# Performance work log

Hardware: AMD Instinct MI355X
Metric: run time of the kernel (lower is better)

The kernel has to match this reference:

```python
import jax, jax.numpy as jnp
import numpy as np

B, T, D, H, V = 512, 128, 1024, 1024, 256
STEPS = 26  # batch_max_length (25) + 1


def setup_inputs() -> dict:
    key = jax.random.key(0)
    ks = jax.random.split(key, 12)
    s = lambda *sh: 1.0 / np.sqrt(sh[-1])
    inp = {
        "batch_H": jax.random.normal(ks[0], (B, T, D), dtype=jnp.float32),
        "text": jax.random.randint(ks[1], (B, STEPS), 0, V, dtype=jnp.int64),
        # AttentionCell params
        "i2h_w": jax.random.normal(ks[2], (H, D), dtype=jnp.float32) * s(H, D),
        "h2h_w": jax.random.normal(ks[3], (H, H), dtype=jnp.float32) * s(H, H),
        "h2h_b": jnp.zeros((H,), dtype=jnp.float32),
        "score_w": jax.random.normal(ks[4], (1, H), dtype=jnp.float32) * s(1, H),
        # LSTMCell params (input = context[D] ++ onehot[V])
        "W_ih": jax.random.normal(ks[5], (4 * H, D + V), dtype=jnp.float32) * s(4 * H, D + V),
        "W_hh": jax.random.normal(ks[6], (4 * H, H), dtype=jnp.float32) * s(4 * H, H),
        "b_ih": jnp.zeros((4 * H,), dtype=jnp.float32),
        "b_hh": jnp.zeros((4 * H,), dtype=jnp.float32),
        # generator
        "gen_w": jax.random.normal(ks[7], (V, H), dtype=jnp.float32) * s(V, H),
        "gen_b": jnp.zeros((V,), dtype=jnp.float32),
    }
    return inp


def reference(batch_H, text, i2h_w, h2h_w, h2h_b, score_w, W_ih, W_hh, b_ih, b_hh, gen_w, gen_b):
    # proj_H = i2h(batch_H): step-invariant, hoisted out of the loop (same math)
    proj_H = jnp.einsum("btd,hd->bth", batch_H, i2h_w)  # [B,T,H]
    dtype = batch_H.dtype

    def step(carry, tok):
        h, c = carry
        # Bahdanau additive attention
        proj_h = h @ h2h_w.T + h2h_b                       # [B,H]
        e = jnp.tanh(proj_H + proj_h[:, None, :]) @ score_w[0]  # [B,T]
        alpha = jax.nn.softmax(e, axis=1)                   # [B,T]
        context = jnp.einsum("bt,btd->bd", alpha, batch_H)  # [B,D]
        x = jnp.concatenate([context, jax.nn.one_hot(tok, V, dtype=dtype)], axis=1)
        # LSTMCell (torch gate order: i, f, g, o)
        gates = x @ W_ih.T + b_ih + h @ W_hh.T + b_hh       # [B,4H]
        i_g, f_g, g_g, o_g = jnp.split(gates, 4, axis=1)
        c_new = jax.nn.sigmoid(f_g) * c + jax.nn.sigmoid(i_g) * jnp.tanh(g_g)
        h_new = jax.nn.sigmoid(o_g) * jnp.tanh(c_new)
        return (h_new, c_new), h_new

    h0 = jnp.zeros((B, H), dtype=dtype)
    c0 = jnp.zeros((B, H), dtype=dtype)
    tokens = jnp.swapaxes(text[:, :STEPS], 0, 1)            # [STEPS,B]
    _, out_hid = jax.lax.scan(step, (h0, c0), tokens)       # [STEPS,B,H]
    out_hid = jnp.swapaxes(out_hid, 0, 1)                   # [B,STEPS,H]
    logits = jnp.einsum("bsh,vh->bsv", out_hid, gen_w) + gen_b
    return logits  # [B, STEPS, V]
```

## Files before the change

kernel.cpp:

```cpp
#include <hip/hip_runtime.h>
#include <hip/hip_fp16.h>

#define BB 512
#define TT 128
#define DD 1024
#define HH 1024
#define VV 256
#define SS 26

typedef _Float16 half8 __attribute__((ext_vector_type(8)));
typedef _Float16 half4 __attribute__((ext_vector_type(4)));
typedef float f32x4 __attribute__((ext_vector_type(4)));

__device__ __forceinline__ void cp16(const void* g, void* l) {
    __builtin_amdgcn_global_load_lds(
        (const __attribute__((address_space(1))) void*)g,
        (__attribute__((address_space(3))) void*)l, 16, 0, 0);
}

__device__ __forceinline__ float tanh_fast(float x) {
    float ex = __expf(2.f * x);
    return 1.f - 2.f * __builtin_amdgcn_rcpf(ex + 1.f);
}
__device__ __forceinline__ float sigmoid_fast(float x) {
    return __builtin_amdgcn_rcpf(1.f + __expf(-x));
}

__global__ void cvt_f32_to_f16_v4(const float* __restrict__ src,
                                  _Float16* __restrict__ dst, long n4) {
    long i = (long)blockIdx.x * blockDim.x + threadIdx.x;
    long stride = (long)gridDim.x * blockDim.x;
    for (; i < n4; i += stride) {
        float4 v = ((const float4*)src)[i];
        half4 h;
        h[0] = (_Float16)v.x; h[1] = (_Float16)v.y;
        h[2] = (_Float16)v.z; h[3] = (_Float16)v.w;
        ((half4*)dst)[i] = h;
    }
}

__global__ void build_wcatp(const float* __restrict__ W_ih,
                            const float* __restrict__ W_hh,
                            _Float16* __restrict__ wcatp) {
    int idx = blockIdx.x * 256 + threadIdx.x;
    int c = idx >> 11;
    int k = idx & 2047;
    int g = c >> 6, q = (c >> 4) & 3, jl = c & 15;
    int row = q * 1024 + g * 16 + jl;
    float v = (k < 1024) ? W_ih[(size_t)row * 1280 + k]
                         : W_hh[(size_t)row * 1024 + (k - 1024)];
    wcatp[idx] = (_Float16)v;
}

__global__ void build_onehT(const float* __restrict__ W_ih,
                            float* __restrict__ onehT) {
    int idx = blockIdx.x * 256 + threadIdx.x;
    int v = idx >> 12;
    int g = idx & 4095;
    onehT[idx] = W_ih[(size_t)g * 1280 + 1024 + v];
}

__global__ void build_bsum(const float* __restrict__ b_ih,
                           const float* __restrict__ b_hh,
                           float* __restrict__ bsum) {
    int i = blockIdx.x * 256 + threadIdx.x;
    bsum[i] = b_ih[i] + b_hh[i];
}

template <int MODE, int SWZ>
__global__ __launch_bounds__(256) void gemm_bt(
    const _Float16* __restrict__ A, int lda,
    const _Float16* __restrict__ B, int ldb,
    void* __restrict__ Cp, int ldc, int K, const float* __restrict__ bias) {
    __shared__ __align__(16) _Float16 As[2][128 * 32];
    __shared__ __align__(16) _Float16 Bs[2][128 * 32];

    int bx = blockIdx.x, by = blockIdx.y;
    if (SWZ) {
        int nx = gridDim.x;
        int bid = by * nx + bx;
        int xcd = bid & 7;
        int local = bid >> 3;
        int rows_per_xcd = gridDim.y >> 3;
        bx = local % nx;
        by = xcd * rows_per_xcd + local / nx;
    }
    const int tid  = threadIdx.x;
    const int lane = tid & 63;
    const int wid  = tid >> 6;
    const int wm   = wid >> 1;
    const int wn   = wid & 1;
    const int m0 = by * 128;
    const int n0 = bx * 128;

    f32x4 acc[4][4];
#pragma unroll
    for (int i = 0; i < 4; ++i)
#pragma unroll
        for (int j = 0; j < 4; ++j)
            acc[i][j] = (f32x4){0.f, 0.f, 0.f, 0.f};

    const int row0 = tid >> 2;
    const int ch0  = tid & 3;
    const _Float16* a0 = A + (size_t)(m0 + row0) * lda + ch0 * 8;
    const _Float16* a1 = A + (size_t)(m0 + row0 + 64) * lda + ch0 * 8;
    const _Float16* b0 = B + (size_t)(n0 + row0) * ldb + ch0 * 8;
    const _Float16* b1 = B + (size_t)(n0 + row0 + 64) * ldb + ch0 * 8;

    const int la = lane & 15;
    const int kc = (lane >> 4) * 8;

    auto stage = [&](int buf, int k0) {
        cp16(a0 + k0, &As[buf][tid * 8]);
        cp16(a1 + k0, &As[buf][64 * 32 + tid * 8]);
        cp16(b0 + k0, &Bs[buf][tid * 8]);
        cp16(b1 + k0, &Bs[buf][64 * 32 + tid * 8]);
    };
    auto compute = [&](int buf) {
        half8 af[4], bf[4];
#pragma unroll
        for (int mt = 0; mt < 4; ++mt)
            af[mt] = *(const half8*)(&As[buf][(wm * 64 + mt * 16 + la) * 32 + kc]);
#pragma unroll
        for (int nt = 0; nt < 4; ++nt)
            bf[nt] = *(const half8*)(&Bs[buf][(wn * 64 + nt * 16 + la) * 32 + kc]);
#pragma unroll
        for (int mt = 0; mt < 4; ++mt)
#pragma unroll
            for (int nt = 0; nt < 4; ++nt)
                acc[mt][nt] = __builtin_amdgcn_mfma_f32_16x16x32_f16(
                    af[mt], bf[nt], acc[mt][nt], 0, 0, 0);
    };

    stage(0, 0);
    __syncthreads();
    for (int k0 = 0; k0 < K; k0 += 64) {
        stage(1, k0 + 32);
        compute(0);
        __syncthreads();
        if (k0 + 64 < K) stage(0, k0 + 64);
        compute(1);
        __syncthreads();
    }

#pragma unroll
    for (int mt = 0; mt < 4; ++mt) {
#pragma unroll
        for (int nt = 0; nt < 4; ++nt) {
            int gn = n0 + wn * 64 + nt * 16 + la;
            float bv = bias ? bias[gn] : 0.f;
#pragma unroll
            for (int r = 0; r < 4; ++r) {
                int gm = m0 + wm * 64 + mt * 16 + (lane >> 4) * 4 + r;
                float v = acc[mt][nt][r] + bv;
                if (MODE == 1) {
                    ((_Float16*)Cp)[(size_t)gm * ldc + gn] = (_Float16)v;
                } else {
                    int s = gm >> 9;
                    int b = gm & 511;
                    ((float*)Cp)[((size_t)b * SS + s) * VV + gn] = v;
                }
            }
        }
    }
}

__global__ __launch_bounds__(256) void gemm_ph(
    const _Float16* __restrict__ A, int lda,
    const _Float16* __restrict__ B, int ldb,
    float* __restrict__ C, int ldc, int K, const float* __restrict__ bias) {
    __shared__ __align__(16) _Float16 As[2][16 * 32];
    __shared__ __align__(16) _Float16 Bs[2][64 * 32];
    const int tid  = threadIdx.x;
    const int lane = tid & 63;
    const int wid  = tid >> 6;
    const int m0 = blockIdx.y * 16;
    const int n0 = blockIdx.x * 64;
    const int row = tid >> 2;
    const int ch  = tid & 3;
    const _Float16* ag = A + (size_t)(m0 + (row & 15)) * lda + ch * 8;
    const _Float16* bg = B + (size_t)(n0 + row) * ldb + ch * 8;
    f32x4 acc = (f32x4){0.f, 0.f, 0.f, 0.f};
    const int la = lane & 15;
    const int kc = (lane >> 4) * 8;

    auto stage = [&](int buf, int k0) {
        if (tid < 64) cp16(ag + k0, &As[buf][tid * 8]);
        cp16(bg + k0, &Bs[buf][tid * 8]);
    };
    auto compute = [&](int buf) {
        half8 af = *(const half8*)(&As[buf][la * 32 + kc]);
        half8 bf = *(const half8*)(&Bs[buf][(wid * 16 + la) * 32 + kc]);
        acc = __builtin_amdgcn_mfma_f32_16x16x32_f16(af, bf, acc, 0, 0, 0);
    };

    stage(0, 0);
    __syncthreads();
    for (int k0 = 0; k0 < K; k0 += 64) {
        stage(1, k0 + 32);
        compute(0);
        __syncthreads();
        if (k0 + 64 < K) stage(0, k0 + 64);
        compute(1);
        __syncthreads();
    }

    int gn = n0 + wid * 16 + la;
    float bv = bias[gn];
    int gm0 = m0 + (lane >> 4) * 4;
#pragma unroll
    for (int r = 0; r < 4; ++r)
        C[(size_t)(gm0 + r) * ldc + gn] = acc[r] + bv;
}

__global__ __launch_bounds__(256) void gemm_gates(
    const _Float16* __restrict__ A,
    const _Float16* __restrict__ B,
    const float* __restrict__ bsum,
    const float* __restrict__ onehT,
    const int* __restrict__ text,
    int step,
    float* __restrict__ c,
    _Float16* __restrict__ acat,
    _Float16* __restrict__ hid) {
    __shared__ __align__(16) _Float16 As[2][64 * 32];
    __shared__ __align__(16) _Float16 Bs[2][128 * 32];
    const int tid  = threadIdx.x;
    const int lane = tid & 63;
    const int wid  = tid >> 6;
    const int wm   = wid >> 1;
    const int wn   = wid & 1;
    const int m0 = blockIdx.y * 64;
    const int n0 = blockIdx.x * 128;
    const int K  = 2048;

    f32x4 acc[2][4];
#pragma unroll
    for (int i = 0; i < 2; ++i)
#pragma unroll
        for (int j = 0; j < 4; ++j)
            acc[i][j] = (f32x4){0.f, 0.f, 0.f, 0.f};

    const int row0 = tid >> 2;
    const int ch0  = tid & 3;
    const _Float16* ag  = A + (size_t)(m0 + row0) * 2048 + ch0 * 8;
    const _Float16* bg0 = B + (size_t)(n0 + row0) * 2048 + ch0 * 8;
    const _Float16* bg1 = B + (size_t)(n0 + row0 + 64) * 2048 + ch0 * 8;
    const int la = lane & 15;
    const int kc = (lane >> 4) * 8;

    auto stage = [&](int buf, int k0) {
        cp16(ag + k0, &As[buf][tid * 8]);
        cp16(bg0 + k0, &Bs[buf][tid * 8]);
        cp16(bg1 + k0, &Bs[buf][64 * 32 + tid * 8]);
    };
    auto compute = [&](int buf) {
        half8 af[2], bf[4];
#pragma unroll
        for (int mt = 0; mt < 2; ++mt)
            af[mt] = *(const half8*)(&As[buf][(wm * 32 + mt * 16 + la) * 32 + kc]);
#pragma unroll
        for (int nt = 0; nt < 4; ++nt)
            bf[nt] = *(const half8*)(&Bs[buf][(wn * 64 + nt * 16 + la) * 32 + kc]);
#pragma unroll
        for (int mt = 0; mt < 2; ++mt)
#pragma unroll
            for (int nt = 0; nt < 4; ++nt)
                acc[mt][nt] = __builtin_amdgcn_mfma_f32_16x16x32_f16(
                    af[mt], bf[nt], acc[mt][nt], 0, 0, 0);
    };

    stage(0, 0);
    __syncthreads();
    for (int k0 = 0; k0 < K; k0 += 64) {
        stage(1, k0 + 32);
        compute(0);
        __syncthreads();
        if (k0 + 64 < K) stage(0, k0 + 64);
        compute(1);
        __syncthreads();
    }

    const int quad = lane >> 4;
    const int jb = (n0 >> 2) + wn * 16 + la;
    float bs[4];
#pragma unroll
    for (int q = 0; q < 4; ++q) bs[q] = bsum[q * 1024 + jb];
#pragma unroll
    for (int mt = 0; mt < 2; ++mt) {
#pragma unroll
        for (int r = 0; r < 4; ++r) {
            int b = m0 + wm * 32 + mt * 16 + quad * 4 + r;
            int tok = text[b * SS + step];
            const float* orow = onehT + (size_t)tok * 4096;
            float ig = acc[mt][0][r] + bs[0] + orow[jb];
            float fg = acc[mt][1][r] + bs[1] + orow[1024 + jb];
            float gg = acc[mt][2][r] + bs[2] + orow[2048 + jb];
            float og = acc[mt][3][r] + bs[3] + orow[3072 + jb];
            size_t ci = (size_t)b * 1024 + jb;
            float cn = sigmoid_fast(fg) * c[ci] + sigmoid_fast(ig) * tanh_fast(gg);
            float hn = sigmoid_fast(og) * tanh_fast(cn);
            c[ci] = cn;
            _Float16 h16 = (_Float16)hn;
            acat[(size_t)b * 2048 + 1024 + jb] = h16;
            hid[((size_t)step * BB + b) * HH + jb] = h16;
        }
    }
}

__global__ __launch_bounds__(512) void attn_kernel(
    const _Float16* __restrict__ pH,
    const _Float16* __restrict__ bh,
    const float* __restrict__ ph,
    const float* __restrict__ sw,
    _Float16* __restrict__ acat) {
    __shared__ float e_s[TT];
    __shared__ float al_s[TT];
    __shared__ __align__(16) float pc[2][DD];

    const int b = blockIdx.x;
    const int tid = threadIdx.x;
    const int lane = tid & 63;
    const int wv = tid >> 6;

    float phr[16], swr[16];
    const float4* ph4 = (const float4*)(ph + (size_t)b * HH + lane * 16);
    const float4* sw4 = (const float4*)(sw + lane * 16);
#pragma unroll
    for (int q = 0; q < 4; ++q) {
        float4 t1 = ph4[q];
        phr[q * 4 + 0] = t1.x; phr[q * 4 + 1] = t1.y;
        phr[q * 4 + 2] = t1.z; phr[q * 4 + 3] = t1.w;
        float4 t2 = sw4[q];
        swr[q * 4 + 0] = t2.x; swr[q * 4 + 1] = t2.y;
        swr[q * 4 + 2] = t2.z; swr[q * 4 + 3] = t2.w;
    }

    const _Float16* pHb = pH + (size_t)b * TT * HH + lane * 16;
#pragma unroll 2
    for (int tt = 0; tt < 16; ++tt) {
        int t = wv * 16 + tt;
        half8 p0 = *(const half8*)(pHb + (size_t)t * HH);
        half8 p1 = *(const half8*)(pHb + (size_t)t * HH + 8);
        float acc = 0.f;
#pragma unroll
        for (int k = 0; k < 8; ++k)
            acc += tanh_fast((float)p0[k] + phr[k]) * swr[k];
#pragma unroll
        for (int k = 0; k < 8; ++k)
            acc += tanh_fast((float)p1[k] + phr[8 + k]) * swr[8 + k];
#pragma unroll
        for (int off = 32; off > 0; off >>= 1) acc += __shfl_xor(acc, off, 64);
        if (lane == 0) e_s[t] = acc;
    }
    __syncthreads();

    if (tid < TT) {
        float m = -1e30f;
        for (int t = 0; t < TT; ++t) m = fmaxf(m, e_s[t]);
        float s = 0.f;
        for (int t = 0; t < TT; ++t) s += __expf(e_s[t] - m);
        al_s[tid] = __expf(e_s[tid] - m) / s;
    }
    __syncthreads();

    const int w2 = tid >> 8;
    const int lc = tid & 255;
    const _Float16* bhb = bh + (size_t)b * TT * DD + lc * 4;
    float c0 = 0.f, c1 = 0.f, c2 = 0.f, c3 = 0.f;
#pragma unroll 8
    for (int t = w2 * 64; t < w2 * 64 + 64; ++t) {
        float a = al_s[t];
        half4 v = *(const half4*)(bhb + (size_t)t * DD);
        c0 += a * (float)v[0];
        c1 += a * (float)v[1];
        c2 += a * (float)v[2];
        c3 += a * (float)v[3];
    }
    ((float4*)pc[w2])[lc] = make_float4(c0, c1, c2, c3);
    __syncthreads();

    if (tid < 256) {
        float4 x0 = ((const float4*)pc[0])[tid];
        float4 x1 = ((const float4*)pc[1])[tid];
        half4 o;
        o[0] = (_Float16)(x0.x + x1.x);
        o[1] = (_Float16)(x0.y + x1.y);
        o[2] = (_Float16)(x0.z + x1.z);
        o[3] = (_Float16)(x0.w + x1.w);
        *(half4*)(acat + (size_t)b * 2048 + tid * 4) = o;
    }
}

extern "C" void kernel_launch(void* const* d_in, const int* in_sizes, int n_in,
                              void* d_out, int out_size, void* d_ws, size_t ws_size,
                              hipStream_t stream) {
    const float* batch_H = (const float*)d_in[0];
    const int*   text    = (const int*)d_in[1];
    const float* i2h_w   = (const float*)d_in[2];
    const float* h2h_w   = (const float*)d_in[3];
    const float* h2h_b   = (const float*)d_in[4];
    const float* score_w = (const float*)d_in[5];
    const float* W_ih    = (const float*)d_in[6];
    const float* W_hh    = (const float*)d_in[7];
    const float* b_ih    = (const float*)d_in[8];
    const float* b_hh    = (const float*)d_in[9];
    const float* gen_w   = (const float*)d_in[10];
    const float* gen_b   = (const float*)d_in[11];
    float* out = (float*)d_out;

    char* ws = (char*)d_ws;
    size_t off = 0;
    auto carve = [&](size_t bytes) -> void* {
        void* p = ws + off;
        off += (bytes + 255) & ~(size_t)255;
        return p;
    };
    _Float16* bh16   = (_Float16*)carve((size_t)BB * TT * DD * 2);
    _Float16* pH16   = (_Float16*)carve((size_t)BB * TT * HH * 2);
    _Float16* wi2h16 = (_Float16*)carve((size_t)HH * DD * 2);
    _Float16* wh2h16 = (_Float16*)carve((size_t)HH * HH * 2);
    _Float16* wcatp  = (_Float16*)carve((size_t)4 * HH * 2048 * 2);
    _Float16* wgen16 = (_Float16*)carve((size_t)VV * HH * 2);
    float*    onehT  = (float*)carve((size_t)VV * 4 * HH * 4);
    float*    bsum   = (float*)carve((size_t)4 * HH * 4);
    _Float16* acat   = (_Float16*)carve((size_t)BB * 2048 * 2);
    float*    ph_f   = (float*)carve((size_t)BB * HH * 4);
    float*    c_f    = (float*)carve((size_t)BB * HH * 4);
    _Float16* hid16  = (_Float16*)carve((size_t)SS * BB * HH * 2);

    const dim3 blk(256);

    cvt_f32_to_f16_v4<<<dim3(16384), blk, 0, stream>>>(batch_H, bh16, (long)BB * TT * DD / 4);
    cvt_f32_to_f16_v4<<<dim3(1024), blk, 0, stream>>>(i2h_w, wi2h16, (long)HH * DD / 4);
    cvt_f32_to_f16_v4<<<dim3(1024), blk, 0, stream>>>(h2h_w, wh2h16, (long)HH * HH / 4);
    cvt_f32_to_f16_v4<<<dim3(256), blk, 0, stream>>>(gen_w, wgen16, (long)VV * HH / 4);
    build_wcatp<<<dim3(4 * HH * 2048 / 256), blk, 0, stream>>>(W_ih, W_hh, wcatp);
    build_onehT<<<dim3(VV * 4 * HH / 256), blk, 0, stream>>>(W_ih, onehT);
    build_bsum<<<dim3(16), blk, 0, stream>>>(b_ih, b_hh, bsum);
    hipMemsetAsync(acat, 0, (size_t)BB * 2048 * 2, stream);
    hipMemsetAsync(c_f, 0, (size_t)BB * HH * 4, stream);

    for (int i = 0; i < 8; ++i) {
        gemm_bt<1, 1><<<dim3(HH / 128, BB * TT / 128 / 8), blk, 0, stream>>>(
            bh16 + (size_t)i * (BB * TT / 8) * DD, DD, wi2h16, DD,
            pH16 + (size_t)i * (BB * TT / 8) * HH, HH, DD, nullptr);
    }

    for (int s = 0; s < SS; ++s) {
        gemm_ph<<<dim3(HH / 64, BB / 16), blk, 0, stream>>>(
            acat + 1024, 2048, wh2h16, HH, ph_f, HH, HH, h2h_b);

        attn_kernel<<<dim3(BB), dim3(512), 0, stream>>>(pH16, bh16, ph_f, score_w, acat);

        gemm_gates<<<dim3(4 * HH / 128, BB / 64), blk, 0, stream>>>(
            acat, wcatp, bsum, onehT, text, s, c_f, acat, hid16);
    }

    gemm_bt<2, 0><<<dim3(VV / 128, SS * BB / 128), blk, 0, stream>>>(
        hid16, HH, wgen16, HH, out, VV, HH, gen_b);
}
```

Before: 3.606 ms.

## Shrink gates GEMM tile, parallelize softmax, widen context loads, merge i2h launches

The gates GEMM tile drops from 64x128 to 64x64, doubling the grid from 256 to 512 blocks to fill more CUs at the cost of less reuse per block. The attention kernel computes its softmax with a wave-shuffle reduction instead of every thread looping serially over 128 scores. The context reduction now uses half8 loads across four partial groups. The eight chunked i2h projection GEMM launches are merged into a single launch.

```diff
diff --git a/kernel.cpp b/kernel.cpp
--- a/kernel.cpp
+++ b/kernel.cpp
@@ -224,50 +224,39 @@
     _Float16* __restrict__ acat,
     _Float16* __restrict__ hid) {
     __shared__ __align__(16) _Float16 As[2][64 * 32];
-    __shared__ __align__(16) _Float16 Bs[2][128 * 32];
+    __shared__ __align__(16) _Float16 Bs[2][64 * 32];
     const int tid  = threadIdx.x;
     const int lane = tid & 63;
     const int wid  = tid >> 6;
-    const int wm   = wid >> 1;
-    const int wn   = wid & 1;
     const int m0 = blockIdx.y * 64;
-    const int n0 = blockIdx.x * 128;
+    const int n0 = blockIdx.x * 64;
     const int K  = 2048;
 
-    f32x4 acc[2][4];
-#pragma unroll
-    for (int i = 0; i < 2; ++i)
-#pragma unroll
-        for (int j = 0; j < 4; ++j)
-            acc[i][j] = (f32x4){0.f, 0.f, 0.f, 0.f};
+    f32x4 acc[4];
+#pragma unroll
+    for (int j = 0; j < 4; ++j) acc[j] = (f32x4){0.f, 0.f, 0.f, 0.f};
 
     const int row0 = tid >> 2;
     const int ch0  = tid & 3;
-    const _Float16* ag  = A + (size_t)(m0 + row0) * 2048 + ch0 * 8;
-    const _Float16* bg0 = B + (size_t)(n0 + row0) * 2048 + ch0 * 8;
-    const _Float16* bg1 = B + (size_t)(n0 + row0 + 64) * 2048 + ch0 * 8;
+    const _Float16* ag = A + (size_t)(m0 + row0) * 2048 + ch0 * 8;
+    const _Float16* bg = B + (size_t)(n0 + row0) * 2048 + ch0 * 8;
     const int la = lane & 15;
     const int kc = (lane >> 4) * 8;
 
     auto stage = [&](int buf, int k0) {
         cp16(ag + k0, &As[buf][tid * 8]);
-        cp16(bg0 + k0, &Bs[buf][tid * 8]);
-        cp16(bg1 + k0, &Bs[buf][64 * 32 + tid * 8]);
+        cp16(bg + k0, &Bs[buf][tid * 8]);
     };
     auto compute = [&](int buf) {
-        half8 af[2], bf[4];
-#pragma unroll
-        for (int mt = 0; mt < 2; ++mt)
-            af[mt] = *(const half8*)(&As[buf][(wm * 32 + mt * 16 + la) * 32 + kc]);
+        half8 af = *(const half8*)(&As[buf][(wid * 16 + la) * 32 + kc]);
+        half8 bf[4];
 #pragma unroll
         for (int nt = 0; nt < 4; ++nt)
-            bf[nt] = *(const half8*)(&Bs[buf][(wn * 64 + nt * 16 + la) * 32 + kc]);
-#pragma unroll
-        for (int mt = 0; mt < 2; ++mt)
-#pragma unroll
-            for (int nt = 0; nt < 4; ++nt)
-                acc[mt][nt] = __builtin_amdgcn_mfma_f32_16x16x32_f16(
-                    af[mt], bf[nt], acc[mt][nt], 0, 0, 0);
+            bf[nt] = *(const half8*)(&Bs[buf][(nt * 16 + la) * 32 + kc]);
+#pragma unroll
+        for (int nt = 0; nt < 4; ++nt)
+            acc[nt] = __builtin_amdgcn_mfma_f32_16x16x32_f16(
+                af, bf[nt], acc[nt], 0, 0, 0);
     };
 
     stage(0, 0);
@@ -282,29 +271,26 @@
     }
 
     const int quad = lane >> 4;
-    const int jb = (n0 >> 2) + wn * 16 + la;
+    const int jb = (n0 >> 2) + la;
     float bs[4];
 #pragma unroll
     for (int q = 0; q < 4; ++q) bs[q] = bsum[q * 1024 + jb];
 #pragma unroll
-    for (int mt = 0; mt < 2; ++mt) {
-#pragma unroll
-        for (int r = 0; r < 4; ++r) {
-            int b = m0 + wm * 32 + mt * 16 + quad * 4 + r;
-            int tok = text[b * SS + step];
-            const float* orow = onehT + (size_t)tok * 4096;
-            float ig = acc[mt][0][r] + bs[0] + orow[jb];
-            float fg = acc[mt][1][r] + bs[1] + orow[1024 + jb];
-            float gg = acc[mt][2][r] + bs[2] + orow[2048 + jb];
-            float og = acc[mt][3][r] + bs[3] + orow[3072 + jb];
-            size_t ci = (size_t)b * 1024 + jb;
-            float cn = sigmoid_fast(fg) * c[ci] + sigmoid_fast(ig) * tanh_fast(gg);
-            float hn = sigmoid_fast(og) * tanh_fast(cn);
-            c[ci] = cn;
-            _Float16 h16 = (_Float16)hn;
-            acat[(size_t)b * 2048 + 1024 + jb] = h16;
-            hid[((size_t)step * BB + b) * HH + jb] = h16;
-        }
+    for (int r = 0; r < 4; ++r) {
+        int b = m0 + wid * 16 + quad * 4 + r;
+        int tok = text[b * SS + step];
+        const float* orow = onehT + (size_t)tok * 4096;
+        float ig = acc[0][r] + bs[0] + orow[jb];
+        float fg = acc[1][r] + bs[1] + orow[1024 + jb];
+        float gg = acc[2][r] + bs[2] + orow[2048 + jb];
+        float og = acc[3][r] + bs[3] + orow[3072 + jb];
+        size_t ci = (size_t)b * 1024 + jb;
+        float cn = sigmoid_fast(fg) * c[ci] + sigmoid_fast(ig) * tanh_fast(gg);
+        float hn = sigmoid_fast(og) * tanh_fast(cn);
+        c[ci] = cn;
+        _Float16 h16 = (_Float16)hn;
+        acat[(size_t)b * 2048 + 1024 + jb] = h16;
+        hid[((size_t)step * BB + b) * HH + jb] = h16;
     }
 }
 
@@ -316,7 +302,7 @@
     _Float16* __restrict__ acat) {
     __shared__ float e_s[TT];
     __shared__ float al_s[TT];
-    __shared__ __align__(16) float pc[2][DD];
+    __shared__ __align__(16) float4 pc2[4][2][128];
 
     const int b = blockIdx.x;
     const int tid = threadIdx.x;
@@ -355,39 +341,58 @@
     }
     __syncthreads();
 
-    if (tid < TT) {
-        float m = -1e30f;
-        for (int t = 0; t < TT; ++t) m = fmaxf(m, e_s[t]);
-        float s = 0.f;
-        for (int t = 0; t < TT; ++t) s += __expf(e_s[t] - m);
-        al_s[tid] = __expf(e_s[tid] - m) / s;
-    }
-    __syncthreads();
-
-    const int w2 = tid >> 8;
-    const int lc = tid & 255;
-    const _Float16* bhb = bh + (size_t)b * TT * DD + lc * 4;
+    if (tid < 64) {
+        float e0 = e_s[tid];
+        float e1 = e_s[64 + tid];
+        float m = fmaxf(e0, e1);
+#pragma unroll
+        for (int off = 32; off > 0; off >>= 1)
+            m = fmaxf(m, __shfl_xor(m, off, 64));
+        float x0 = __expf(e0 - m);
+        float x1 = __expf(e1 - m);
+        float ssum = x0 + x1;
+#pragma unroll
+        for (int off = 32; off > 0; off >>= 1)
+            ssum += __shfl_xor(ssum, off, 64);
+        float inv = __builtin_amdgcn_rcpf(ssum);
+        al_s[tid] = x0 * inv;
+        al_s[64 + tid] = x1 * inv;
+    }
+    __syncthreads();
+
+    const int w4 = tid >> 7;
+    const int lc = tid & 127;
+    const _Float16* bhb = bh + (size_t)b * TT * DD + lc * 8;
     float c0 = 0.f, c1 = 0.f, c2 = 0.f, c3 = 0.f;
-#pragma unroll 8
-    for (int t = w2 * 64; t < w2 * 64 + 64; ++t) {
+    float c4 = 0.f, c5 = 0.f, c6 = 0.f, c7 = 0.f;
+#pragma unroll 4
+    for (int t = w4 * 32; t < w4 * 32 + 32; ++t) {
         float a = al_s[t];
-        half4 v = *(const half4*)(bhb + (size_t)t * DD);
+        half8 v = *(const half8*)(bhb + (size_t)t * DD);
         c0 += a * (float)v[0];
         c1 += a * (float)v[1];
         c2 += a * (float)v[2];
         c3 += a * (float)v[3];
-    }
-    ((float4*)pc[w2])[lc] = make_float4(c0, c1, c2, c3);
+        c4 += a * (float)v[4];
+        c5 += a * (float)v[5];
+        c6 += a * (float)v[6];
+        c7 += a * (float)v[7];
+    }
+    pc2[w4][0][lc] = make_float4(c0, c1, c2, c3);
+    pc2[w4][1][lc] = make_float4(c4, c5, c6, c7);
     __syncthreads();
 
     if (tid < 256) {
-        float4 x0 = ((const float4*)pc[0])[tid];
-        float4 x1 = ((const float4*)pc[1])[tid];
+        int hf = tid & 1, slot = tid >> 1;
+        float4 s0 = pc2[0][hf][slot];
+        float4 s1 = pc2[1][hf][slot];
+        float4 s2 = pc2[2][hf][slot];
+        float4 s3 = pc2[3][hf][slot];
         half4 o;
-        o[0] = (_Float16)(x0.x + x1.x);
-        o[1] = (_Float16)(x0.y + x1.y);
-        o[2] = (_Float16)(x0.z + x1.z);
-        o[3] = (_Float16)(x0.w + x1.w);
+        o[0] = (_Float16)(s0.x + s1.x + s2.x + s3.x);
+        o[1] = (_Float16)(s0.y + s1.y + s2.y + s3.y);
+        o[2] = (_Float16)(s0.z + s1.z + s2.z + s3.z);
+        o[3] = (_Float16)(s0.w + s1.w + s2.w + s3.w);
         *(half4*)(acat + (size_t)b * 2048 + tid * 4) = o;
     }
 }
@@ -441,11 +446,8 @@
     hipMemsetAsync(acat, 0, (size_t)BB * 2048 * 2, stream);
     hipMemsetAsync(c_f, 0, (size_t)BB * HH * 4, stream);
 
-    for (int i = 0; i < 8; ++i) {
-        gemm_bt<1, 1><<<dim3(HH / 128, BB * TT / 128 / 8), blk, 0, stream>>>(
-            bh16 + (size_t)i * (BB * TT / 8) * DD, DD, wi2h16, DD,
-            pH16 + (size_t)i * (BB * TT / 8) * HH, HH, DD, nullptr);
-    }
+    gemm_bt<1, 1><<<dim3(HH / 128, BB * TT / 128), blk, 0, stream>>>(
+        bh16, DD, wi2h16, DD, pH16, HH, DD, nullptr);
 
     for (int s = 0; s < SS; ++s) {
         gemm_ph<<<dim3(HH / 64, BB / 16), blk, 0, stream>>>(
@@ -453,7 +455,7 @@
 
         attn_kernel<<<dim3(BB), dim3(512), 0, stream>>>(pH16, bh16, ph_f, score_w, acat);
 
-        gemm_gates<<<dim3(4 * HH / 128, BB / 64), blk, 0, stream>>>(
+        gemm_gates<<<dim3(4 * HH / 64, BB / 64), blk, 0, stream>>>(
             acat, wcatp, bsum, onehT, text, s, c_f, acat, hid16);
     }
 
```

After: 3.297 ms. 8.6% less time.
